# Optimization experiments

Measured on AMD Instinct MI355X. Metric: run time of the kernel, lower is better.

## Reference

```python
import jax, jax.numpy as jnp
import numpy as np

B, N = 1, 2048
C_REF, C_ATOM, C_PAIR = 389, 128, 16


def setup_inputs() -> dict:
    key = jax.random.key(0)
    ks = jax.random.split(key, 12)
    inp = {
        "ref_pos": jax.random.normal(ks[0], (B, N, 3), jnp.float32),
        "ref_charge": jax.random.normal(ks[1], (B, N), jnp.float32),
        "ref_mask": jnp.ones((B, N), jnp.float32),
        "ref_element": jax.random.uniform(ks[2], (B, N, 128), jnp.float32),
        "ref_atom_name_chars": jax.random.uniform(ks[3], (B, N, 4, 64), jnp.float32),
        "ref_space_uid": jax.random.randint(ks[4], (B, N), 0, 256, jnp.int32),
        # learned params (fan-in scaled init)
        "W_feats": jax.random.normal(ks[5], (C_REF, C_ATOM), jnp.float32) / np.sqrt(C_REF),
        "b_feats": jnp.zeros((C_ATOM,), jnp.float32),
        "W_off": jax.random.normal(ks[6], (3, C_PAIR), jnp.float32) / np.sqrt(3.0),
        "b_off": jnp.zeros((C_PAIR,), jnp.float32),
        "W_inv": jax.random.normal(ks[7], (1, C_PAIR), jnp.float32),
        "b_inv": jnp.zeros((C_PAIR,), jnp.float32),
        "W_vm": jax.random.normal(ks[8], (1, C_PAIR), jnp.float32),
        "b_vm": jnp.zeros((C_PAIR,), jnp.float32),
    }
    return inp


def reference(ref_pos, ref_charge, ref_mask, ref_element, ref_atom_name_chars,
              ref_space_uid, W_feats, b_feats, W_off, b_off, W_inv, b_inv,
              W_vm, b_vm):
    # --- atom single conditioning cl: [B, N, c_atom] ---
    names_flat = ref_atom_name_chars.reshape(*ref_atom_name_chars.shape[:-2], -1)  # [B,N,256]
    feats = jnp.concatenate(
        [ref_pos, ref_charge[..., None], ref_mask[..., None], ref_element, names_flat],
        axis=-1)  # [B,N,389]
    cl = feats @ W_feats + b_feats

    # --- atom pair conditioning plm: [B, N, N, c_atom_pair] ---
    dlm = ref_pos[..., :, None, :] - ref_pos[..., None, :, :]  # [B,N,N,3]
    vlm = (ref_space_uid[..., None, :] == ref_space_uid[..., :, None]).astype(dlm.dtype)  # [B,N,N]
    v = vlm[..., None]  # [B,N,N,1]

    plm = (dlm @ W_off + b_off) * v
    inv_sq = 1.0 / (1.0 + jnp.sum(dlm * dlm, axis=-1, keepdims=True))  # [B,N,N,1]
    plm = plm + (inv_sq @ W_inv + b_inv) * v
    plm = plm + (v @ W_vm + b_vm) * v
    return cl, plm
```

## Files before the change

kernel.cpp:

```cpp
#include <hip/hip_runtime.h>

#define NN 2048
#define CA 128
#define CR 389
#define CP 16

__global__ __launch_bounds__(256) void fused_kernel(
    const float* __restrict__ pos, const float* __restrict__ charge,
    const float* __restrict__ mask, const float* __restrict__ elem,
    const float* __restrict__ names, const float* __restrict__ Wf,
    const float* __restrict__ bfeats,
    const int* __restrict__ uid,
    const float* __restrict__ Woff, const float* __restrict__ boff,
    const float* __restrict__ Winv, const float* __restrict__ binv,
    const float* __restrict__ Wvm, const float* __restrict__ bvm,
    float* __restrict__ cl, float* __restrict__ plm)
{
    __shared__ float ft[8][CR];
    const int tid = threadIdx.x;

    if (blockIdx.x < NN) {
        const int q = tid & 3;
        const int p = tid >> 2;

        float w0[4], w1[4], w2[4], wi[4], kk[4];
        #pragma unroll
        for (int i = 0; i < 4; ++i) {
            int c = q * 4 + i;
            w0[i] = Woff[c];
            w1[i] = Woff[CP + c];
            w2[i] = Woff[2 * CP + c];
            wi[i] = Winv[c];
            kk[i] = Wvm[c] + boff[c] + binv[c] + bvm[c];
        }

        const int l = blockIdx.x;
        const float plx = pos[l * 3 + 0];
        const float ply = pos[l * 3 + 1];
        const float plz = pos[l * 3 + 2];
        const int ul = uid[l];
        float4* __restrict__ dst = (float4*)(plm + (size_t)l * NN * CP);

        #pragma unroll 4
        for (int j = 0; j < NN / 64; ++j) {
            const int m = j * 64 + p;
            const float dx = plx - pos[m * 3 + 0];
            const float dy = ply - pos[m * 3 + 1];
            const float dz = plz - pos[m * 3 + 2];
            const float inv = 1.0f / (1.0f + dx * dx + dy * dy + dz * dz);
            const unsigned sel = (uid[m] == ul) ? 0xFFFFFFFFu : 0u;

            float rx = fmaf(dx, w0[0], fmaf(dy, w1[0], fmaf(dz, w2[0], fmaf(inv, wi[0], kk[0]))));
            float ry = fmaf(dx, w0[1], fmaf(dy, w1[1], fmaf(dz, w2[1], fmaf(inv, wi[1], kk[1]))));
            float rz = fmaf(dx, w0[2], fmaf(dy, w1[2], fmaf(dz, w2[2], fmaf(inv, wi[2], kk[2]))));
            float rw = fmaf(dx, w0[3], fmaf(dy, w1[3], fmaf(dz, w2[3], fmaf(inv, wi[3], kk[3]))));

            float4 r;
            r.x = __uint_as_float(__float_as_uint(rx) & sel);
            r.y = __uint_as_float(__float_as_uint(ry) & sel);
            r.z = __uint_as_float(__float_as_uint(rz) & sel);
            r.w = __uint_as_float(__float_as_uint(rw) & sel);

            dst[j * 256 + tid] = r;
        }
    } else {
        const int n0 = (blockIdx.x - NN) * 8;

        for (int idx = tid; idx < 8 * CR; idx += 256) {
            int a = idx / CR;
            int k = idx - a * CR;
            int n = n0 + a;
            float v;
            if (k < 3)         v = pos[n * 3 + k];
            else if (k == 3)   v = charge[n];
            else if (k == 4)   v = mask[n];
            else if (k < 133)  v = elem[n * 128 + (k - 5)];
            else               v = names[n * 256 + (k - 133)];
            ft[a][k] = v;
        }
        __syncthreads();

        const int c = tid & 127;
        const int half = tid >> 7;
        float a0 = 0.f, a1 = 0.f, a2 = 0.f, a3 = 0.f;
        #pragma unroll 4
        for (int k = 0; k < CR; ++k) {
            const float w = Wf[k * CA + c];
            a0 = fmaf(ft[half * 4 + 0][k], w, a0);
            a1 = fmaf(ft[half * 4 + 1][k], w, a1);
            a2 = fmaf(ft[half * 4 + 2][k], w, a2);
            a3 = fmaf(ft[half * 4 + 3][k], w, a3);
        }
        const float bb = bfeats[c];
        const int nb = n0 + half * 4;
        cl[(size_t)(nb + 0) * CA + c] = a0 + bb;
        cl[(size_t)(nb + 1) * CA + c] = a1 + bb;
        cl[(size_t)(nb + 2) * CA + c] = a2 + bb;
        cl[(size_t)(nb + 3) * CA + c] = a3 + bb;
    }
}

extern "C" void kernel_launch(void* const* d_in, const int* in_sizes, int n_in,
                              void* d_out, int out_size, void* d_ws, size_t ws_size,
                              hipStream_t stream)
{
    const float* pos    = (const float*)d_in[0];
    const float* charge = (const float*)d_in[1];
    const float* mask   = (const float*)d_in[2];
    const float* elem   = (const float*)d_in[3];
    const float* names  = (const float*)d_in[4];
    const int*   uid    = (const int*)  d_in[5];
    const float* Wf     = (const float*)d_in[6];
    const float* bfeats = (const float*)d_in[7];
    const float* Woff   = (const float*)d_in[8];
    const float* boff   = (const float*)d_in[9];
    const float* Winv   = (const float*)d_in[10];
    const float* binv   = (const float*)d_in[11];
    const float* Wvm    = (const float*)d_in[12];
    const float* bvm    = (const float*)d_in[13];

    float* cl  = (float*)d_out;
    float* plm = (float*)d_out + (size_t)NN * CA;

    fused_kernel<<<NN + NN / 8, 256, 0, stream>>>(
        pos, charge, mask, elem, names, Wf, bfeats, uid,
        Woff, boff, Winv, binv, Wvm, bvm, cl, plm);
}
```

Baseline: 364.4 us.

## Switch plm to persistent grid-stride blocks with per-thread fixed column atom

Replaces the one-block-per-row plm launch (2048 blocks) with 512 persistent blocks that grid-stride over the flattened output. Each thread fixes one column atom m and loads its position and uid once, while the row atom is wave-uniform and read through readfirstlane, which allows scalar loads. The cl blocks are moved to the front of the grid. The goals are less block-launch overhead, fewer per-element vector loads, and cl work overlapping the plm stream. The risk is lower occupancy with 512 blocks of 256 threads, which may not saturate write bandwidth on the MI355X.

```diff
diff --git a/kernel.cpp b/kernel.cpp
--- a/kernel.cpp
+++ b/kernel.cpp
@@ -4,6 +4,12 @@
 #define CA 128
 #define CR 389
 #define CP 16
+
+#define CL_BLOCKS   256
+#define PLM_BLOCKS  512
+#define PLM_G       (PLM_BLOCKS * 256)
+#define PLM_CHUNKS  (NN * NN * CP / 4)
+#define PLM_ITERS   (PLM_CHUNKS / PLM_G)
 
 __global__ __launch_bounds__(256) void fused_kernel(
     const float* __restrict__ pos, const float* __restrict__ charge,
@@ -19,9 +25,11 @@
     __shared__ float ft[8][CR];
     const int tid = threadIdx.x;
 
-    if (blockIdx.x < NN) {
-        const int q = tid & 3;
-        const int p = tid >> 2;
+    if (blockIdx.x >= CL_BLOCKS) {
+        const int g  = (blockIdx.x - CL_BLOCKS) * 256 + tid;
+        const int q  = g & 3;
+        const int mm = (g >> 2) & (NN - 1);
+        const int lb = g >> 13;
 
         float w0[4], w1[4], w2[4], wi[4], kk[4];
         #pragma unroll
@@ -33,22 +41,22 @@
             wi[i] = Winv[c];
             kk[i] = Wvm[c] + boff[c] + binv[c] + bvm[c];
         }
+        const float mx = pos[mm * 3 + 0];
+        const float my = pos[mm * 3 + 1];
+        const float mz = pos[mm * 3 + 2];
+        const int   um = uid[mm];
 
-        const int l = blockIdx.x;
-        const float plx = pos[l * 3 + 0];
-        const float ply = pos[l * 3 + 1];
-        const float plz = pos[l * 3 + 2];
-        const int ul = uid[l];
-        float4* __restrict__ dst = (float4*)(plm + (size_t)l * NN * CP);
+        float4* __restrict__ dst = (float4*)plm;
 
         #pragma unroll 4
-        for (int j = 0; j < NN / 64; ++j) {
-            const int m = j * 64 + p;
-            const float dx = plx - pos[m * 3 + 0];
-            const float dy = ply - pos[m * 3 + 1];
-            const float dz = plz - pos[m * 3 + 2];
+        for (int i = 0; i < PLM_ITERS; ++i) {
+            const int l  = lb + (i << 4);
+            const int lu = __builtin_amdgcn_readfirstlane(l);
+            const float dx = pos[lu * 3 + 0] - mx;
+            const float dy = pos[lu * 3 + 1] - my;
+            const float dz = pos[lu * 3 + 2] - mz;
             const float inv = 1.0f / (1.0f + dx * dx + dy * dy + dz * dz);
-            const unsigned sel = (uid[m] == ul) ? 0xFFFFFFFFu : 0u;
+            const unsigned sel = (uid[lu] == um) ? 0xFFFFFFFFu : 0u;
 
             float rx = fmaf(dx, w0[0], fmaf(dy, w1[0], fmaf(dz, w2[0], fmaf(inv, wi[0], kk[0]))));
             float ry = fmaf(dx, w0[1], fmaf(dy, w1[1], fmaf(dz, w2[1], fmaf(inv, wi[1], kk[1]))));
@@ -61,10 +69,10 @@
             r.z = __uint_as_float(__float_as_uint(rz) & sel);
             r.w = __uint_as_float(__float_as_uint(rw) & sel);
 
-            dst[j * 256 + tid] = r;
+            dst[(unsigned)g + (unsigned)i * PLM_G] = r;
         }
     } else {
-        const int n0 = (blockIdx.x - NN) * 8;
+        const int n0 = blockIdx.x * 8;
 
         for (int idx = tid; idx < 8 * CR; idx += 256) {
             int a = idx / CR;
@@ -122,7 +130,7 @@
     float* cl  = (float*)d_out;
     float* plm = (float*)d_out + (size_t)NN * CA;
 
-    fused_kernel<<<NN + NN / 8, 256, 0, stream>>>(
+    fused_kernel<<<CL_BLOCKS + PLM_BLOCKS, 256, 0, stream>>>(
         pos, charge, mask, elem, names, Wf, bfeats, uid,
         Woff, boff, Winv, binv, Wvm, bvm, cl, plm);
 }
```

New measurement: 352.4 us. 1.03x faster.
